# Performance work log

Hardware: AMD Instinct MI355X
Metric: run time of the kernel (lower is better)

The kernel has to match this reference:

```python
import jax, jax.numpy as jnp
import numpy as np

B, T = 64, 2048
DEC, ENC, ATT, LOC, K = 1024, 512, 128, 32, 31


def setup_inputs() -> dict:
    key = jax.random.key(0)
    ks = jax.random.split(key, 9)
    inv = lambda n: 1.0 / np.sqrt(n)
    return {
        "query": jax.random.normal(ks[0], (B, DEC), dtype=jnp.float32),
        "values": jax.random.normal(ks[1], (B, T, ENC), dtype=jnp.float32),
        "cumulative_attention_weights": jax.random.uniform(ks[2], (B, T), dtype=jnp.float32),
        "mask": jnp.zeros((B, T), dtype=bool),
        "Q_w": jax.random.uniform(ks[3], (ATT, DEC), jnp.float32, -inv(DEC), inv(DEC)),
        "Q_b": jax.random.uniform(ks[4], (ATT,), jnp.float32, -inv(DEC), inv(DEC)),
        "V_w": jax.random.uniform(ks[5], (ATT, ENC), jnp.float32, -inv(ENC), inv(ENC)),
        "conv_w": jax.random.uniform(ks[6], (LOC, 1, K), jnp.float32, -inv(K), inv(K)),
        "loc_proj_w": jax.random.uniform(ks[7], (ATT, LOC), jnp.float32, -inv(LOC), inv(LOC)),
        "v_w": jax.random.uniform(ks[8], (1, ATT), jnp.float32, -inv(ATT), inv(ATT)),
    }


def reference(query, values, cumulative_attention_weights, mask,
              Q_w, Q_b, V_w, conv_w, loc_proj_w, v_w):
    # query projection: [B, 1, ATT] (broadcast over T)
    q = query @ Q_w.T + Q_b                       # [B, ATT]
    q = q[:, None, :]
    # values cache: [B, T, ATT]
    v_cache = jnp.einsum("bte,ae->bta", values, V_w)
    # location features: Conv1d(1 -> LOC, k=31, same padding) over cum weights
    x = cumulative_attention_weights[:, None, :]   # [B, 1, T]
    loc = jax.lax.conv_general_dilated(
        x, conv_w, window_strides=(1,), padding="SAME",
        dimension_numbers=("NCH", "OIH", "NCH"))   # [B, LOC, T]
    loc = jnp.einsum("bct,ac->bta", loc, loc_proj_w)  # [B, T, ATT]
    # additive attention energies
    energies = jnp.tanh(q + v_cache + loc) @ v_w[0]   # [B, T]
    energies = jnp.where(mask, -jnp.inf, energies)
    attention_weights = jax.nn.softmax(energies, axis=1)
    # context: [B, ENC]
    attention_context = jnp.einsum("bt,bte->be", attention_weights, values)
    return attention_context, attention_weights
```

## Files before the change

kernel.cpp:

```cpp
#include <hip/hip_runtime.h>
#include <hip/hip_bf16.h>
#include <math.h>

#define B_  64
#define T_  2048
#define DEC_ 1024
#define ENC_ 512
#define ATT_ 128
#define LOC_ 32
#define KW_  31

typedef __attribute__((ext_vector_type(8))) short short8;
typedef __attribute__((ext_vector_type(4))) float f32x4;

__device__ inline unsigned short bf16_rn(float x) {
    unsigned int u = __builtin_bit_cast(unsigned int, x);
    unsigned int r = u + 0x7fffu + ((u >> 16) & 1u);
    return (unsigned short)(r >> 16);
}
__device__ inline float bf16_to_f(unsigned short h) {
    unsigned int u = ((unsigned int)h) << 16;
    return __builtin_bit_cast(float, u);
}
__device__ inline void cvt_pair(float4 a, float4 b2, short8& hi, short8& lo) {
    float f[8] = {a.x, a.y, a.z, a.w, b2.x, b2.y, b2.z, b2.w};
    #pragma unroll
    for (int j = 0; j < 8; ++j) {
        unsigned short h = bf16_rn(f[j]);
        hi[j] = (short)h;
        lo[j] = (short)bf16_rn(f[j] - bf16_to_f(h));
    }
}

__global__ __launch_bounds__(256) void prep_kernel(
    const float* __restrict__ query, const float* __restrict__ Q_w,
    const float* __restrict__ Q_b, const float* __restrict__ conv_w,
    const float* __restrict__ loc_proj_w, const float* __restrict__ V_w,
    float* __restrict__ qbuf,
    unsigned short* __restrict__ Bph, unsigned short* __restrict__ Bpl,
    unsigned short* __restrict__ effh, unsigned short* __restrict__ effl)
{
    int bi = blockIdx.x, tid = threadIdx.x;
    if (bi < 256) {
        int b = bi >> 2, grp = bi & 3;
        __shared__ float sq[DEC_];
        *(float4*)(&sq[tid * 4]) = *(const float4*)(query + (size_t)b * DEC_ + tid * 4);
        __syncthreads();
        int w = tid >> 6, lane = tid & 63;
        int a0 = grp * 32 + w * 8;
        for (int p = 0; p < 4; ++p) {
            int a = a0 + 2 * p;
            const float* r0 = Q_w + (size_t)a * DEC_;
            const float* r1 = r0 + DEC_;
            float s0 = 0.f, s1 = 0.f;
            #pragma unroll
            for (int i = 0; i < 4; ++i) {
                float4 q0 = *(const float4*)(r0 + i * 256 + lane * 4);
                float4 q1 = *(const float4*)(r1 + i * 256 + lane * 4);
                float4 xq = *(const float4*)(sq + i * 256 + lane * 4);
                s0 += q0.x * xq.x + q0.y * xq.y + q0.z * xq.z + q0.w * xq.w;
                s1 += q1.x * xq.x + q1.y * xq.y + q1.z * xq.z + q1.w * xq.w;
            }
            #pragma unroll
            for (int m = 32; m >= 1; m >>= 1) {
                s0 += __shfl_xor(s0, m, 64);
                s1 += __shfl_xor(s1, m, 64);
            }
            if (lane == 0) {
                qbuf[b * ATT_ + a]     = s0 + Q_b[a];
                qbuf[b * ATT_ + a + 1] = s1 + Q_b[a + 1];
            }
        }
    } else if (bi == 256) {
        __shared__ float slp[ATT_ * LOC_];
        __shared__ float scw[LOC_ * KW_];
        for (int i = tid; i < ATT_ * LOC_; i += 256) slp[i] = loc_proj_w[i];
        for (int i = tid; i < LOC_ * KW_; i += 256) scw[i] = conv_w[i];
        __syncthreads();
        if (tid < ATT_) {
            int n = tid;
            for (int k = 0; k < 32; ++k) {
                float s = 0.f;
                if (k < KW_)
                    #pragma unroll
                    for (int c = 0; c < LOC_; ++c)
                        s += slp[n * LOC_ + c] * scw[c * KW_ + k];
                unsigned short h = bf16_rn(s);
                effh[n * 32 + k] = h;
                effl[n * 32 + k] = bf16_rn(s - bf16_to_f(h));
            }
        }
    } else {
        int g0 = (bi - 257) * 512;
        #pragma unroll
        for (int p = 0; p < 2; ++p) {
            int gi = g0 + p * 256 + tid;
            int n  = gi >> 7;
            int kq = (gi & 127) * 4;
            float4 v = ((const float4*)V_w)[gi];
            ushort4 h4, l4;
            h4.x = bf16_rn(v.x); l4.x = bf16_rn(v.x - bf16_to_f(h4.x));
            h4.y = bf16_rn(v.y); l4.y = bf16_rn(v.y - bf16_to_f(h4.y));
            h4.z = bf16_rn(v.z); l4.z = bf16_rn(v.z - bf16_to_f(h4.z));
            h4.w = bf16_rn(v.w); l4.w = bf16_rn(v.w - bf16_to_f(h4.w));
            int dst = (kq >> 5) * 4096 + n * 32 + (kq & 31);
            *(ushort4*)(Bph + dst) = h4;
            *(ushort4*)(Bpl + dst) = l4;
        }
    }
}

__global__ __launch_bounds__(256, 2) void energy_kernel(
    const float* __restrict__ values, const float* __restrict__ cum,
    const float* __restrict__ qbuf,
    const unsigned short* __restrict__ Bph, const unsigned short* __restrict__ Bpl,
    const unsigned short* __restrict__ effh, const unsigned short* __restrict__ effl,
    const float* __restrict__ vw, float* __restrict__ energies)
{
    __shared__ float sx[160];

    const int tid = threadIdx.x;
    const int bx  = blockIdx.x;
    const int b   = bx >> 4;
    const int t0  = (bx & 15) * 128;

    if (tid < 160) {
        int g = t0 - 15 + tid;
        sx[tid] = (g >= 0 && g < T_) ? cum[b * T_ + g] : 0.f;
    }
    __syncthreads();

    const int w      = tid >> 6;
    const int lane   = tid & 63;
    const int lane15 = lane & 15;
    const int quad   = lane >> 4;

    f32x4 acc[2][8];
    #pragma unroll
    for (int i = 0; i < 2; ++i)
        #pragma unroll
        for (int j = 0; j < 8; ++j) acc[i][j] = (f32x4){0.f, 0.f, 0.f, 0.f};

    const float* abase = values + ((size_t)b * T_ + t0 + w * 32 + lane15) * ENC_ + quad * 8;
    const unsigned short* bbh = Bph + lane15 * 32 + quad * 8;
    const unsigned short* bbl = Bpl + lane15 * 32 + quad * 8;

    float4 pf[2][2];
    #pragma unroll
    for (int i = 0; i < 2; ++i) {
        pf[i][0] = *(const float4*)(abase + i * 16 * ENC_);
        pf[i][1] = *(const float4*)(abase + i * 16 * ENC_ + 4);
    }

    for (int kc = 0; kc < ENC_; kc += 32) {
        short8 ah[2], al[2];
        #pragma unroll
        for (int i = 0; i < 2; ++i) cvt_pair(pf[i][0], pf[i][1], ah[i], al[i]);

        short8 bh[8], bl[8];
        const int chunk = (kc >> 5) * 4096;
        #pragma unroll
        for (int j = 0; j < 8; ++j) {
            bh[j] = *(const short8*)(bbh + chunk + j * 512);
            bl[j] = *(const short8*)(bbl + chunk + j * 512);
        }
        __builtin_amdgcn_sched_barrier(0);
        if (kc + 32 < ENC_) {
            #pragma unroll
            for (int i = 0; i < 2; ++i) {
                pf[i][0] = *(const float4*)(abase + i * 16 * ENC_ + kc + 32);
                pf[i][1] = *(const float4*)(abase + i * 16 * ENC_ + kc + 36);
            }
        }
        __builtin_amdgcn_sched_barrier(0);
        #pragma unroll
        for (int j = 0; j < 8; ++j)
            #pragma unroll
            for (int i = 0; i < 2; ++i) {
                acc[i][j] = __builtin_amdgcn_mfma_f32_16x16x32_bf16(ah[i], bh[j], acc[i][j], 0, 0, 0);
                acc[i][j] = __builtin_amdgcn_mfma_f32_16x16x32_bf16(ah[i], bl[j], acc[i][j], 0, 0, 0);
                acc[i][j] = __builtin_amdgcn_mfma_f32_16x16x32_bf16(al[i], bh[j], acc[i][j], 0, 0, 0);
            }
    }

    {
        short8 ah[2], al[2];
        #pragma unroll
        for (int i = 0; i < 2; ++i) {
            int base = w * 32 + i * 16 + lane15 + quad * 8;
            #pragma unroll
            for (int j2 = 0; j2 < 8; ++j2) {
                float xv = sx[base + j2];
                unsigned short h = bf16_rn(xv);
                ah[i][j2] = (short)h;
                al[i][j2] = (short)bf16_rn(xv - bf16_to_f(h));
            }
        }
        #pragma unroll
        for (int j = 0; j < 8; ++j) {
            int n = j * 16 + lane15;
            short8 bh = *(const short8*)(effh + n * 32 + quad * 8);
            short8 bl = *(const short8*)(effl + n * 32 + quad * 8);
            #pragma unroll
            for (int i = 0; i < 2; ++i) {
                acc[i][j] = __builtin_amdgcn_mfma_f32_16x16x32_bf16(ah[i], bh, acc[i][j], 0, 0, 0);
                acc[i][j] = __builtin_amdgcn_mfma_f32_16x16x32_bf16(ah[i], bl, acc[i][j], 0, 0, 0);
                acc[i][j] = __builtin_amdgcn_mfma_f32_16x16x32_bf16(al[i], bh, acc[i][j], 0, 0, 0);
            }
        }
    }

    float qv[8], vv[8];
    #pragma unroll
    for (int j = 0; j < 8; ++j) {
        int n = j * 16 + lane15;
        qv[j] = qbuf[b * ATT_ + n];
        vv[j] = vw[n];
    }
    #pragma unroll
    for (int i = 0; i < 2; ++i)
        #pragma unroll
        for (int r = 0; r < 4; ++r) {
            float s = 0.f;
            #pragma unroll
            for (int j = 0; j < 8; ++j)
                s += vv[j] * tanhf(acc[i][j][r] + qv[j]);
            #pragma unroll
            for (int m = 8; m >= 1; m >>= 1) s += __shfl_xor(s, m, 64);
            if (lane15 == 0)
                energies[b * T_ + t0 + w * 32 + i * 16 + quad * 4 + r] = s;
        }
}

__global__ __launch_bounds__(256) void softmax_kernel(
    const float* __restrict__ energies, const unsigned char* __restrict__ mask,
    float* __restrict__ out)
{
    int b = blockIdx.x, tid = threadIdx.x;
    float* ctx  = out;
    float* wout = out + B_ * ENC_;

    for (int i = tid; i < ENC_; i += 256) ctx[b * ENC_ + i] = 0.f;

    float e[8];
    float mx = -INFINITY;
    #pragma unroll
    for (int p = 0; p < 8; ++p) {
        int t = p * 256 + tid;
        float v = energies[b * T_ + t];
        if (mask[b * T_ + t]) v = -INFINITY;
        e[p] = v;
        mx = fmaxf(mx, v);
    }
    #pragma unroll
    for (int m = 32; m >= 1; m >>= 1) mx = fmaxf(mx, __shfl_xor(mx, m, 64));
    __shared__ float red[8];
    int wave = tid >> 6;
    if ((tid & 63) == 0) red[wave] = mx;
    __syncthreads();
    mx = fmaxf(fmaxf(red[0], red[1]), fmaxf(red[2], red[3]));

    float sum = 0.f;
    #pragma unroll
    for (int p = 0; p < 8; ++p) {
        e[p] = expf(e[p] - mx);
        sum += e[p];
    }
    #pragma unroll
    for (int m = 32; m >= 1; m >>= 1) sum += __shfl_xor(sum, m, 64);
    if ((tid & 63) == 0) red[4 + wave] = sum;
    __syncthreads();
    sum = red[4] + red[5] + red[6] + red[7];
    float inv = 1.f / sum;
    #pragma unroll
    for (int p = 0; p < 8; ++p)
        wout[b * T_ + p * 256 + tid] = e[p] * inv;
}

__global__ __launch_bounds__(256) void context_kernel(
    const float* __restrict__ values, const float* __restrict__ w,
    float* __restrict__ ctx)
{
    int bx = blockIdx.x;
    int b = bx >> 5, seg = bx & 31;
    int tid = threadIdx.x;
    int tt = tid >> 7;
    int e4 = (tid & 127) * 4;

    __shared__ float sw[64];
    if (tid < 64) sw[tid] = w[b * T_ + seg * 64 + tid];
    __syncthreads();

    const float* vp = values + ((size_t)b * T_ + seg * 64) * ENC_ + e4;
    float4 acc = make_float4(0.f, 0.f, 0.f, 0.f);
    #pragma unroll 8
    for (int t = tt * 32; t < tt * 32 + 32; ++t) {
        float4 v = *(const float4*)(vp + (size_t)t * ENC_);
        float wv = sw[t];
        acc.x += wv * v.x; acc.y += wv * v.y;
        acc.z += wv * v.z; acc.w += wv * v.w;
    }

    __shared__ float red[512];
    if (tt == 1) *(float4*)&red[e4] = acc;
    __syncthreads();
    if (tt == 0) {
        float4 o = *(const float4*)&red[e4];
        atomicAdd(&ctx[b * ENC_ + e4 + 0], acc.x + o.x);
        atomicAdd(&ctx[b * ENC_ + e4 + 1], acc.y + o.y);
        atomicAdd(&ctx[b * ENC_ + e4 + 2], acc.z + o.z);
        atomicAdd(&ctx[b * ENC_ + e4 + 3], acc.w + o.w);
    }
}

extern "C" void kernel_launch(void* const* d_in, const int* in_sizes, int n_in,
                              void* d_out, int out_size, void* d_ws, size_t ws_size,
                              hipStream_t stream) {
    const float* query        = (const float*)d_in[0];
    const float* values       = (const float*)d_in[1];
    const float* cum          = (const float*)d_in[2];
    const unsigned char* mask = (const unsigned char*)d_in[3];
    const float* Q_w          = (const float*)d_in[4];
    const float* Q_b          = (const float*)d_in[5];
    const float* V_w          = (const float*)d_in[6];
    const float* conv_w       = (const float*)d_in[7];
    const float* loc_proj_w   = (const float*)d_in[8];
    const float* v_w          = (const float*)d_in[9];

    float* out = (float*)d_out;
    char*  ws  = (char*)d_ws;
    float*          qbuf     = (float*)(ws);
    unsigned short* Bph      = (unsigned short*)(ws + 32768);
    unsigned short* Bpl      = (unsigned short*)(ws + 163840);
    unsigned short* effh     = (unsigned short*)(ws + 294912);
    unsigned short* effl     = (unsigned short*)(ws + 303104);
    float*          energies = (float*)(ws + 311296);

    prep_kernel<<<289, 256, 0, stream>>>(query, Q_w, Q_b, conv_w, loc_proj_w, V_w,
                                         qbuf, Bph, Bpl, effh, effl);
    energy_kernel<<<1024, 256, 0, stream>>>(values, cum, qbuf, Bph, Bpl,
                                            effh, effl, v_w, energies);
    softmax_kernel<<<B_, 256, 0, stream>>>(energies, mask, out);
    context_kernel<<<B_ * 32, 256, 0, stream>>>(values, out + B_ * ENC_, out);
}
```

Measured before the change: 477.2 us.

## Fuse softmax and context into energy kernel using split-softmax partial statistics

The energy kernel now computes a block-local softmax (max and sum) over its 128 timesteps and immediately does the weighted sum over values for that tile, writing per-block context partials and stats. A small combine kernel rescales the partials with the global max and sum to produce the final context and weights. The aim is to avoid re-reading the 256MB values tensor in a separate context pass while the tile is likely still in cache, and to remove two kernel launches and the atomics. The cost is extra register and shared-memory pressure in the energy kernel and an extra workspace buffer.

```diff
diff --git a/kernel.cpp b/kernel.cpp
--- a/kernel.cpp
+++ b/kernel.cpp
@@ -110,14 +110,18 @@
     }
 }
 
-__global__ __launch_bounds__(256, 2) void energy_kernel(
+__global__ __launch_bounds__(256, 2) void energy_ctx_kernel(
     const float* __restrict__ values, const float* __restrict__ cum,
     const float* __restrict__ qbuf,
     const unsigned short* __restrict__ Bph, const unsigned short* __restrict__ Bpl,
     const unsigned short* __restrict__ effh, const unsigned short* __restrict__ effl,
-    const float* __restrict__ vw, float* __restrict__ energies)
+    const float* __restrict__ vw, const unsigned char* __restrict__ mask,
+    float* __restrict__ wU, float* __restrict__ bstats,
+    float* __restrict__ ctxpart)
 {
     __shared__ float sx[160];
+    __shared__ float se[128];
+    __shared__ float red[512];
 
     const int tid = threadIdx.x;
     const int bx  = blockIdx.x;
@@ -228,88 +232,96 @@
             #pragma unroll
             for (int m = 8; m >= 1; m >>= 1) s += __shfl_xor(s, m, 64);
             if (lane15 == 0)
-                energies[b * T_ + t0 + w * 32 + i * 16 + quad * 4 + r] = s;
-        }
-}
-
-__global__ __launch_bounds__(256) void softmax_kernel(
-    const float* __restrict__ energies, const unsigned char* __restrict__ mask,
-    float* __restrict__ out)
+                se[w * 32 + i * 16 + quad * 4 + r] = s;
+        }
+    __syncthreads();
+
+    if (tid < 128 && mask[b * T_ + t0 + tid]) se[tid] = -INFINITY;
+    __syncthreads();
+
+    float e0 = se[lane * 2], e1 = se[lane * 2 + 1];
+    float mx = fmaxf(e0, e1);
+    #pragma unroll
+    for (int m = 32; m >= 1; m >>= 1) mx = fmaxf(mx, __shfl_xor(mx, m, 64));
+    float w0 = 0.f, w1 = 0.f;
+    if (mx > -INFINITY) {
+        w0 = expf(e0 - mx);
+        w1 = expf(e1 - mx);
+    }
+    float sm = w0 + w1;
+    #pragma unroll
+    for (int m = 32; m >= 1; m >>= 1) sm += __shfl_xor(sm, m, 64);
+    __syncthreads();
+
+    if (w == 0) {
+        se[lane * 2]     = w0;
+        se[lane * 2 + 1] = w1;
+        *(float2*)(wU + b * T_ + t0 + lane * 2) = make_float2(w0, w1);
+        if (lane == 0)
+            *(float2*)(bstats + bx * 2) = make_float2(mx, sm);
+    }
+    __syncthreads();
+
+    {
+        int tt = tid >> 7;
+        int e4 = (tid & 127) * 4;
+        const float* vp = values + ((size_t)b * T_ + t0 + tt * 64) * ENC_ + e4;
+        float4 cacc = make_float4(0.f, 0.f, 0.f, 0.f);
+        #pragma unroll 8
+        for (int t = 0; t < 64; ++t) {
+            float4 v = *(const float4*)(vp + (size_t)t * ENC_);
+            float wv = se[tt * 64 + t];
+            cacc.x += wv * v.x; cacc.y += wv * v.y;
+            cacc.z += wv * v.z; cacc.w += wv * v.w;
+        }
+        if (tt == 1) *(float4*)&red[e4] = cacc;
+        __syncthreads();
+        if (tt == 0) {
+            float4 o = *(const float4*)&red[e4];
+            float4 tot = make_float4(cacc.x + o.x, cacc.y + o.y,
+                                     cacc.z + o.z, cacc.w + o.w);
+            *(float4*)(ctxpart + (size_t)bx * ENC_ + e4) = tot;
+        }
+    }
+}
+
+__global__ __launch_bounds__(256) void combine_kernel(
+    const float* __restrict__ bstats, const float* __restrict__ ctxpart,
+    const float* __restrict__ wU, float* __restrict__ out)
 {
     int b = blockIdx.x, tid = threadIdx.x;
+    __shared__ float smx[16], ssm[16], ssc[16];
+    if (tid < 16) {
+        float2 st = *(const float2*)(bstats + (b * 16 + tid) * 2);
+        smx[tid] = st.x; ssm[tid] = st.y;
+    }
+    __syncthreads();
+    float M = -INFINITY;
+    #pragma unroll
+    for (int k = 0; k < 16; ++k) M = fmaxf(M, smx[k]);
+    if (tid < 16)
+        ssc[tid] = (smx[tid] > -INFINITY) ? expf(smx[tid] - M) : 0.f;
+    __syncthreads();
+    float S = 0.f;
+    #pragma unroll
+    for (int k = 0; k < 16; ++k) S += ssm[k] * ssc[k];
+    float invS = 1.f / S;
+
     float* ctx  = out;
     float* wout = out + B_ * ENC_;
 
-    for (int i = tid; i < ENC_; i += 256) ctx[b * ENC_ + i] = 0.f;
-
-    float e[8];
-    float mx = -INFINITY;
+    float cx = 0.f, cy = 0.f;
+    #pragma unroll
+    for (int k = 0; k < 16; ++k) {
+        float2 v = *(const float2*)(ctxpart + (size_t)(b * 16 + k) * ENC_ + tid * 2);
+        cx += v.x * ssc[k]; cy += v.y * ssc[k];
+    }
+    *(float2*)(ctx + b * ENC_ + tid * 2) = make_float2(cx * invS, cy * invS);
+
     #pragma unroll
     for (int p = 0; p < 8; ++p) {
         int t = p * 256 + tid;
-        float v = energies[b * T_ + t];
-        if (mask[b * T_ + t]) v = -INFINITY;
-        e[p] = v;
-        mx = fmaxf(mx, v);
-    }
-    #pragma unroll
-    for (int m = 32; m >= 1; m >>= 1) mx = fmaxf(mx, __shfl_xor(mx, m, 64));
-    __shared__ float red[8];
-    int wave = tid >> 6;
-    if ((tid & 63) == 0) red[wave] = mx;
-    __syncthreads();
-    mx = fmaxf(fmaxf(red[0], red[1]), fmaxf(red[2], red[3]));
-
-    float sum = 0.f;
-    #pragma unroll
-    for (int p = 0; p < 8; ++p) {
-        e[p] = expf(e[p] - mx);
-        sum += e[p];
-    }
-    #pragma unroll
-    for (int m = 32; m >= 1; m >>= 1) sum += __shfl_xor(sum, m, 64);
-    if ((tid & 63) == 0) red[4 + wave] = sum;
-    __syncthreads();
-    sum = red[4] + red[5] + red[6] + red[7];
-    float inv = 1.f / sum;
-    #pragma unroll
-    for (int p = 0; p < 8; ++p)
-        wout[b * T_ + p * 256 + tid] = e[p] * inv;
-}
-
-__global__ __launch_bounds__(256) void context_kernel(
-    const float* __restrict__ values, const float* __restrict__ w,
-    float* __restrict__ ctx)
-{
-    int bx = blockIdx.x;
-    int b = bx >> 5, seg = bx & 31;
-    int tid = threadIdx.x;
-    int tt = tid >> 7;
-    int e4 = (tid & 127) * 4;
-
-    __shared__ float sw[64];
-    if (tid < 64) sw[tid] = w[b * T_ + seg * 64 + tid];
-    __syncthreads();
-
-    const float* vp = values + ((size_t)b * T_ + seg * 64) * ENC_ + e4;
-    float4 acc = make_float4(0.f, 0.f, 0.f, 0.f);
-    #pragma unroll 8
-    for (int t = tt * 32; t < tt * 32 + 32; ++t) {
-        float4 v = *(const float4*)(vp + (size_t)t * ENC_);
-        float wv = sw[t];
-        acc.x += wv * v.x; acc.y += wv * v.y;
-        acc.z += wv * v.z; acc.w += wv * v.w;
-    }
-
-    __shared__ float red[512];
-    if (tt == 1) *(float4*)&red[e4] = acc;
-    __syncthreads();
-    if (tt == 0) {
-        float4 o = *(const float4*)&red[e4];
-        atomicAdd(&ctx[b * ENC_ + e4 + 0], acc.x + o.x);
-        atomicAdd(&ctx[b * ENC_ + e4 + 1], acc.y + o.y);
-        atomicAdd(&ctx[b * ENC_ + e4 + 2], acc.z + o.z);
-        atomicAdd(&ctx[b * ENC_ + e4 + 3], acc.w + o.w);
+        wout[b * T_ + t] = wU[b * T_ + t] * ssc[t >> 7] * invS;
     }
 }
 
@@ -334,12 +346,14 @@
     unsigned short* Bpl      = (unsigned short*)(ws + 163840);
     unsigned short* effh     = (unsigned short*)(ws + 294912);
     unsigned short* effl     = (unsigned short*)(ws + 303104);
-    float*          energies = (float*)(ws + 311296);
+    float*          wU       = (float*)(ws + 311296);
+    float*          bstats   = (float*)(ws + 835584);
+    float*          ctxpart  = (float*)(ws + 843776);
 
     prep_kernel<<<289, 256, 0, stream>>>(query, Q_w, Q_b, conv_w, loc_proj_w, V_w,
                                          qbuf, Bph, Bpl, effh, effl);
-    energy_kernel<<<1024, 256, 0, stream>>>(values, cum, qbuf, Bph, Bpl,
-                                            effh, effl, v_w, energies);
-    softmax_kernel<<<B_, 256, 0, stream>>>(energies, mask, out);
-    context_kernel<<<B_ * 32, 256, 0, stream>>>(values, out + B_ * ENC_, out);
-}
+    energy_ctx_kernel<<<1024, 256, 0, stream>>>(values, cum, qbuf, Bph, Bpl,
+                                                effh, effl, v_w, mask,
+                                                wU, bstats, ctxpart);
+    combine_kernel<<<B_, 256, 0, stream>>>(bstats, ctxpart, wU, out);
+}
```

Result: faster. 459.4 us, median of 2 (-3.7%).
